# Optimization experiments

Measured on AMD Instinct MI355X. Metric: run time of the kernel, lower is better.

## Reference

```python
import jax, jax.numpy as jnp
import numpy as np

PATCH = 8
C1 = 0.0001
C2 = 0.001


def setup_inputs() -> dict:
    key = jax.random.key(0)
    k1, k2 = jax.random.split(key)
    I1 = jax.random.uniform(k1, (32, 3, 512, 512), dtype=jnp.float32)
    I2 = jax.random.uniform(k2, (32, 3, 512, 512), dtype=jnp.float32)
    return {"I1": I1, "I2": I2}


def reference(I1, I2):
    # Original loops over (b, c); compute_ssim reduces over ALL patches of a
    # channel jointly -> equivalent to global stats over the image cropped to a
    # multiple of the patch size. Output: [B, C].
    p = PATCH
    B, C, H, W = I1.shape
    lp = p if H >= p else H
    Hc, Wc = (H // lp) * lp, (W // lp) * lp
    x = I1[:, :, :Hc, :Wc]
    y = I2[:, :, :Hc, :Wc]
    n = Hc * Wc  # number of elements per (b, c)
    mu1 = x.mean(axis=(2, 3))  # [B, C]
    mu2 = y.mean(axis=(2, 3))
    dx = x - mu1[:, :, None, None]
    dy = y - mu2[:, :, None, None]
    # torch .var() is unbiased (ddof=1)
    sigma1 = (dx * dx).sum(axis=(2, 3)) / (n - 1)
    sigma2 = (dy * dy).sum(axis=(2, 3)) / (n - 1)
    # covariance term uses biased mean, as in the original
    sigma12 = (dx * dy).mean(axis=(2, 3))
    num = (2.0 * mu1 * mu2 + C1) * (2.0 * sigma12 + C2)
    den = (mu1 ** 2 + mu2 ** 2 + C1) * (sigma1 + sigma2 + C2)
    return num / den
```

## Files before the change

### kernel.cpp

```cpp
#include <hip/hip_runtime.h>


#define N_CH 96
#define CH_F4 65536
#define BLOCKS_PER_CH 32
#define BLK_F4 2048
#define THREADS 256
#define ITERS 8

__global__ __launch_bounds__(THREADS) void ssim_partial_kernel(
    const float4* __restrict__ I1, const float4* __restrict__ I2,
    float* __restrict__ ws)
{
    const int gid = blockIdx.x;
    const int ch  = gid >> 5;
    const int blk = gid & 31;
    const long base = (long)ch * CH_F4 + (long)blk * BLK_F4;
    const int t = threadIdx.x;

    float sx = 0.f, sy = 0.f, sxx = 0.f, syy = 0.f, sxy = 0.f;

#pragma unroll
    for (int i = 0; i < ITERS; ++i) {
        float4 a = I1[base + t + i * THREADS];
        float4 b = I2[base + t + i * THREADS];
        sx  += a.x + a.y + a.z + a.w;
        sy  += b.x + b.y + b.z + b.w;
        sxx += a.x * a.x + a.y * a.y + a.z * a.z + a.w * a.w;
        syy += b.x * b.x + b.y * b.y + b.z * b.z + b.w * b.w;
        sxy += a.x * b.x + a.y * b.y + a.z * b.z + a.w * b.w;
    }

#pragma unroll
    for (int off = 32; off > 0; off >>= 1) {
        sx  += __shfl_down(sx,  off);
        sy  += __shfl_down(sy,  off);
        sxx += __shfl_down(sxx, off);
        syy += __shfl_down(syy, off);
        sxy += __shfl_down(sxy, off);
    }

    __shared__ float red[4][5];
    const int wave = t >> 6;
    const int lane = t & 63;
    if (lane == 0) {
        red[wave][0] = sx;  red[wave][1] = sy;  red[wave][2] = sxx;
        red[wave][3] = syy; red[wave][4] = sxy;
    }
    __syncthreads();
    if (t == 0) {
        float* o = ws + (size_t)gid * 5;
        o[0] = red[0][0] + red[1][0] + red[2][0] + red[3][0];
        o[1] = red[0][1] + red[1][1] + red[2][1] + red[3][1];
        o[2] = red[0][2] + red[1][2] + red[2][2] + red[3][2];
        o[3] = red[0][3] + red[1][3] + red[2][3] + red[3][3];
        o[4] = red[0][4] + red[1][4] + red[2][4] + red[3][4];
    }
}

__global__ __launch_bounds__(64) void ssim_final_kernel(
    const float* __restrict__ ws, float* __restrict__ out)
{
    const int ch   = blockIdx.x;
    const int lane = threadIdx.x;

    float sx = 0.f, sy = 0.f, sxx = 0.f, syy = 0.f, sxy = 0.f;
    if (lane < BLOCKS_PER_CH) {
        const float* p = ws + ((size_t)ch * BLOCKS_PER_CH + lane) * 5;
        sx = p[0]; sy = p[1]; sxx = p[2]; syy = p[3]; sxy = p[4];
    }
#pragma unroll
    for (int off = 16; off > 0; off >>= 1) {
        sx  += __shfl_down(sx,  off);
        sy  += __shfl_down(sy,  off);
        sxx += __shfl_down(sxx, off);
        syy += __shfl_down(syy, off);
        sxy += __shfl_down(sxy, off);
    }
    if (lane == 0) {
        const double n  = 262144.0;
        const double C1 = 0.0001, C2 = 0.001;
        double Sx = sx, Sy = sy, Sxx = sxx, Syy = syy, Sxy = sxy;
        double mu1 = Sx / n;
        double mu2 = Sy / n;
        double s1  = (Sxx - Sx * Sx / n) / (n - 1.0);
        double s2  = (Syy - Sy * Sy / n) / (n - 1.0);
        double s12 = (Sxy - Sx * Sy / n) / n;
        double num = (2.0 * mu1 * mu2 + C1) * (2.0 * s12 + C2);
        double den = (mu1 * mu1 + mu2 * mu2 + C1) * (s1 + s2 + C2);
        out[ch] = (float)(num / den);
    }
}

extern "C" void kernel_launch(void* const* d_in, const int* in_sizes, int n_in,
                              void* d_out, int out_size, void* d_ws, size_t ws_size,
                              hipStream_t stream)
{
    const float4* I1 = (const float4*)d_in[0];
    const float4* I2 = (const float4*)d_in[1];
    float* ws  = (float*)d_ws;
    float* out = (float*)d_out;

    ssim_partial_kernel<<<N_CH * BLOCKS_PER_CH, THREADS, 0, stream>>>(I1, I2, ws);
    ssim_final_kernel<<<N_CH, 64, 0, stream>>>(ws, out);
}
```

Before: 35.60 us.

## Fuse final reduction into partial kernel via last-block atomic counter

Merges the two-kernel reduction into a single kernel: each block writes its partials, increments a global atomic counter, and the last block to finish reduces all channels in double precision and writes the SSIM outputs. It also halves the blocks per channel and doubles the loads each thread does. The aim is to remove the second kernel launch, but it adds a memset launch, a serial tail done by one block, and fewer blocks to hide memory latency.

```diff
diff --git a/kernel.cpp b/kernel.cpp
--- a/kernel.cpp
+++ b/kernel.cpp
@@ -1,21 +1,24 @@
 #include <hip/hip_runtime.h>
 
 
-#define N_CH 96
-#define CH_F4 65536
-#define BLOCKS_PER_CH 32
-#define BLK_F4 2048
+#define N_CH    96
+#define CH_F4   65536
+#define BPC     16
 #define THREADS 256
-#define ITERS 8
+#define ITERS   16
 
-__global__ __launch_bounds__(THREADS) void ssim_partial_kernel(
+#define NBLOCKS (N_CH * BPC)
+#define CNT_OFF (NBLOCKS * 5)
+
+__global__ __launch_bounds__(THREADS) void ssim_fused_kernel(
     const float4* __restrict__ I1, const float4* __restrict__ I2,
-    float* __restrict__ ws)
+    float* __restrict__ ws, unsigned int* __restrict__ counter,
+    float* __restrict__ out)
 {
     const int gid = blockIdx.x;
-    const int ch  = gid >> 5;
-    const int blk = gid & 31;
-    const long base = (long)ch * CH_F4 + (long)blk * BLK_F4;
+    const int ch  = gid >> 4;
+    const int blk = gid & (BPC - 1);
+    const long base = (long)ch * CH_F4 + (long)blk * (THREADS * ITERS);
     const int t = threadIdx.x;
 
     float sx = 0.f, sy = 0.f, sxx = 0.f, syy = 0.f, sxy = 0.f;
@@ -41,6 +44,7 @@
     }
 
     __shared__ float red[4][5];
+    __shared__ bool  amLast;
     const int wave = t >> 6;
     const int lane = t & 63;
     if (lane == 0) {
@@ -55,40 +59,36 @@
         o[2] = red[0][2] + red[1][2] + red[2][2] + red[3][2];
         o[3] = red[0][3] + red[1][3] + red[2][3] + red[3][3];
         o[4] = red[0][4] + red[1][4] + red[2][4] + red[3][4];
+        __threadfence();
+        unsigned int done = atomicAdd(counter, 1u);
+        amLast = (done == NBLOCKS - 1);
     }
-}
+    __syncthreads();
 
-__global__ __launch_bounds__(64) void ssim_final_kernel(
-    const float* __restrict__ ws, float* __restrict__ out)
-{
-    const int ch   = blockIdx.x;
-    const int lane = threadIdx.x;
-
-    float sx = 0.f, sy = 0.f, sxx = 0.f, syy = 0.f, sxy = 0.f;
-    if (lane < BLOCKS_PER_CH) {
-        const float* p = ws + ((size_t)ch * BLOCKS_PER_CH + lane) * 5;
-        sx = p[0]; sy = p[1]; sxx = p[2]; syy = p[3]; sxy = p[4];
-    }
+    if (amLast) {
+        __threadfence();
+        if (t < N_CH) {
+            double Sx = 0.0, Sy = 0.0, Sxx = 0.0, Syy = 0.0, Sxy = 0.0;
+            const float* p = ws + (size_t)t * BPC * 5;
 #pragma unroll
-    for (int off = 16; off > 0; off >>= 1) {
-        sx  += __shfl_down(sx,  off);
-        sy  += __shfl_down(sy,  off);
-        sxx += __shfl_down(sxx, off);
-        syy += __shfl_down(syy, off);
-        sxy += __shfl_down(sxy, off);
-    }
-    if (lane == 0) {
-        const double n  = 262144.0;
-        const double C1 = 0.0001, C2 = 0.001;
-        double Sx = sx, Sy = sy, Sxx = sxx, Syy = syy, Sxy = sxy;
-        double mu1 = Sx / n;
-        double mu2 = Sy / n;
-        double s1  = (Sxx - Sx * Sx / n) / (n - 1.0);
-        double s2  = (Syy - Sy * Sy / n) / (n - 1.0);
-        double s12 = (Sxy - Sx * Sy / n) / n;
-        double num = (2.0 * mu1 * mu2 + C1) * (2.0 * s12 + C2);
-        double den = (mu1 * mu1 + mu2 * mu2 + C1) * (s1 + s2 + C2);
-        out[ch] = (float)(num / den);
+            for (int b = 0; b < BPC; ++b) {
+                Sx  += (double)p[b * 5 + 0];
+                Sy  += (double)p[b * 5 + 1];
+                Sxx += (double)p[b * 5 + 2];
+                Syy += (double)p[b * 5 + 3];
+                Sxy += (double)p[b * 5 + 4];
+            }
+            const double n  = 262144.0;
+            const double C1 = 0.0001, C2 = 0.001;
+            double mu1 = Sx / n;
+            double mu2 = Sy / n;
+            double s1  = (Sxx - Sx * Sx / n) / (n - 1.0);
+            double s2  = (Syy - Sy * Sy / n) / (n - 1.0);
+            double s12 = (Sxy - Sx * Sy / n) / n;
+            double num = (2.0 * mu1 * mu2 + C1) * (2.0 * s12 + C2);
+            double den = (mu1 * mu1 + mu2 * mu2 + C1) * (s1 + s2 + C2);
+            out[t] = (float)(num / den);
+        }
     }
 }
 
@@ -99,8 +99,10 @@
     const float4* I1 = (const float4*)d_in[0];
     const float4* I2 = (const float4*)d_in[1];
     float* ws  = (float*)d_ws;
+    unsigned int* counter = (unsigned int*)(ws + CNT_OFF);
     float* out = (float*)d_out;
 
-    ssim_partial_kernel<<<N_CH * BLOCKS_PER_CH, THREADS, 0, stream>>>(I1, I2, ws);
-    ssim_final_kernel<<<N_CH, 64, 0, stream>>>(ws, out);
+    hipMemsetAsync(counter, 0, sizeof(unsigned int), stream);
+
+    ssim_fused_kernel<<<NBLOCKS, THREADS, 0, stream>>>(I1, I2, ws, counter, out);
 }
```

Measured after the change: 87.68 us. 146% more time.
